# Performance work log

Measured on AMD Instinct MI355X. Metric: run time of the kernel, lower is better.

The kernel has to match this reference:

```python
import itertools
import jax, jax.numpy as jnp
import numpy as np

B, RES = 256, 16
DIM, KEY_DIM, NUM_HEADS, ATTN_RATIO = 448, 32, 8, 4
SEQ = RES * RES
EXP_KEY_DIM = ATTN_RATIO * KEY_DIM          # 128
TOTAL_KEY = KEY_DIM * NUM_HEADS             # 256
TOTAL_EXP = EXP_KEY_DIM * NUM_HEADS         # 1024
QKV_DIM = TOTAL_EXP + 2 * TOTAL_KEY         # 1536
SCALE = KEY_DIM ** -0.5


def _build_bias_idxs():
    # Replicates the itertools.product loop from build()
    points = list(itertools.product(range(RES), range(RES)))
    offsets = {}
    idxs = []
    for p1 in points:
        for p2 in points:
            off = (abs(p1[0] - p2[0]), abs(p1[1] - p2[1]))
            if off not in offsets:
                offsets[off] = len(offsets)
            idxs.append(offsets[off])
    return np.asarray(idxs, dtype=np.int32).reshape(SEQ, SEQ), len(offsets)


def setup_inputs() -> dict:
    key = jax.random.key(0)
    ks = jax.random.split(key, 6)
    bias_idxs_np, n_off = _build_bias_idxs()
    std = 0.02
    return {
        "hidden_states": jax.random.normal(ks[0], (B, SEQ, DIM), dtype=jnp.float32),
        "qkv_w": jax.random.normal(ks[1], (DIM, QKV_DIM), dtype=jnp.float32) * std,
        "qkv_b": jnp.zeros((QKV_DIM,), dtype=jnp.float32),
        "proj_w": jax.random.normal(ks[2], (TOTAL_EXP, DIM), dtype=jnp.float32) * std,
        "proj_b": jnp.zeros((DIM,), dtype=jnp.float32),
        "attention_biases": jax.random.normal(ks[3], (NUM_HEADS, n_off), dtype=jnp.float32) * std,
        "attention_bias_idxs": jnp.asarray(bias_idxs_np),
    }


def reference(hidden_states, qkv_w, qkv_b, proj_w, proj_b, attention_biases, attention_bias_idxs):
    b, s, _ = hidden_states.shape
    qkv = hidden_states @ qkv_w + qkv_b                       # [B,S,1536]
    qkv = qkv.reshape(b, s, NUM_HEADS, KEY_DIM * 2 + EXP_KEY_DIM)
    q, k, v = jnp.split(qkv, [KEY_DIM, 2 * KEY_DIM], axis=3)  # [B,S,H,dk],[B,S,H,dk],[B,S,H,dv]
    scores = jnp.einsum("bqhd,bkhd->bhqk", q, k) * SCALE      # [B,H,S,S]
    bias = attention_biases[:, attention_bias_idxs]           # [H,S,S] gather
    probs = jax.nn.softmax(scores + bias[None], axis=-1)
    ctx = jnp.einsum("bhqk,bkhd->bqhd", probs, v)             # [B,S,H,dv]
    ctx = ctx.reshape(b, s, TOTAL_EXP)
    return ctx @ proj_w + proj_b
```

## Files before the change

### kernel.cpp

```cpp
#include <hip/hip_runtime.h>
#include <hip/hip_bf16.h>
#include <stdint.h>


typedef __attribute__((ext_vector_type(4))) float f32x4;
typedef __attribute__((ext_vector_type(8))) short short8;
typedef __attribute__((ext_vector_type(4))) unsigned short u16x4;
typedef __attribute__((ext_vector_type(2))) unsigned int u32x2;

#define DEVINL static __device__ __forceinline__

DEVINL unsigned short f2bf(float f) {
  unsigned u = __float_as_uint(f);
  return (unsigned short)((u + 0x7FFFu + ((u >> 16) & 1u)) >> 16);
}
DEVINL float bf2f(short s) {
  return __uint_as_float(((unsigned)(unsigned short)s) << 16);
}
DEVINL unsigned cvt_pk_bf16(float lo, float hi) {
  unsigned r;
  asm("v_cvt_pk_bf16_f32 %0, %1, %2" : "=v"(r) : "v"(lo), "v"(hi));
  return r;
}

DEVINL void gload_lds16(const void* g, void* l) {
  __builtin_amdgcn_global_load_lds((const __attribute__((address_space(1))) void*)g,
                                   (__attribute__((address_space(3))) void*)l,
                                   16, 0, 0);
}

#define SCALE 0.17677669529663687f
#define LOG2E 1.4426950408889634f

#define WS_XB     ((size_t)0)
#define WS_CTX    ((size_t)0)
#define WS_WQT    ((size_t)134217728)
#define WS_WPT    ((size_t)135593984)
#define WS_QW     ((size_t)136642560)
#define WS_KW     ((size_t)170196992)
#define WS_VT     ((size_t)203751424)
#define WS_QKVBP  ((size_t)342163456)

DEVINL int qkv_perm(int np, float* sc) {
  *sc = 1.0f;
  if (np < 512) {
    const int h = np >> 6, c = np & 63;
    if (c < 32) *sc = SCALE * LOG2E;
    return h * 192 + c;
  }
  const int h = (np - 512) >> 7, e = (np - 512) & 127;
  return h * 192 + 64 + e;
}


__global__ void k_convert_x(const float* __restrict__ x, short* __restrict__ xb) {
  const size_t i = (size_t)blockIdx.x * blockDim.x + threadIdx.x;
  const f32x4* src = (const f32x4*)x + i * 2;
  f32x4 a = src[0], b = src[1];
  short8 o;
#pragma unroll
  for (int t = 0; t < 4; ++t) o[t] = (short)f2bf(a[t]);
#pragma unroll
  for (int t = 0; t < 4; ++t) o[4 + t] = (short)f2bf(b[t]);
  ((short8*)xb)[i] = o;
}

__global__ void k_prep_qkvw(const float* __restrict__ w, short* __restrict__ out) {
  const int idx = blockIdx.x * blockDim.x + threadIdx.x;
  if (idx >= 1536 * 448) return;
  const int np = idx / 448, k = idx - np * 448;
  float sc;
  const int n = qkv_perm(np, &sc);
  out[idx] = (short)f2bf(w[(size_t)k * 1536 + n] * sc);
}

__global__ void k_prep_qkvb(const float* __restrict__ bsrc, float* __restrict__ bdst) {
  const int np = blockIdx.x * blockDim.x + threadIdx.x;
  if (np >= 1536) return;
  float sc;
  const int n = qkv_perm(np, &sc);
  bdst[np] = bsrc[n] * sc;
}

__global__ void k_transpose_bf16(const float* __restrict__ in, short* __restrict__ out,
                                 int K, int N, int total) {
  const int idx = blockIdx.x * blockDim.x + threadIdx.x;
  if (idx >= total) return;
  const int n = idx / K, k = idx - n * K;
  const float v = (n < N) ? in[(size_t)k * N + n] : 0.0f;
  out[idx] = (short)f2bf(v);
}


template <int KSTEPS, int LDA, int LDB, bool SWAP>
DEVINL void gemm128_pipe3(const short* __restrict__ A, const short* __restrict__ B,
                          short* Asm , short* Bsm ,
                          int m0, int n0, int tid, f32x4 acc[4][4]) {
  const int lane = tid & 63, wave = tid >> 6;
  const int l15 = lane & 15, g = lane >> 4;
  const int wm = wave >> 1, wn = wave & 1;
  const int r8 = lane >> 3;
  const int scol = (((lane & 7) ^ r8) << 3);
  const int wbase = wave * 32;

  const short* Ab = A + (size_t)(m0 + wbase + r8) * LDA + scol;
  const short* Bb = B + (size_t)(n0 + wbase + r8) * LDB + scol;

  auto stageA = [&](int k) {
    short* dst = Asm + (k % 3) * 8192 + wbase * 64;
    const short* src = Ab + (size_t)k * 64;
#pragma unroll
    for (int c = 0; c < 4; ++c) gload_lds16(src + (size_t)(c * 8) * LDA, dst + c * 512);
  };
  auto stageB = [&](int k) {
    short* dst = Bsm + (k % 2) * 8192 + wbase * 64;
    const short* src = Bb + (size_t)k * 64;
#pragma unroll
    for (int c = 0; c < 4; ++c) gload_lds16(src + (size_t)(c * 8) * LDB, dst + c * 512);
  };
  auto compute = [&](int k) {
    const short* Ac = Asm + (k % 3) * 8192;
    const short* Bc = Bsm + (k % 2) * 8192;
#pragma unroll
    for (int s = 0; s < 2; ++s) {
      const int rslot = (((s * 4 + g) ^ (l15 & 7)) << 3);
      short8 a[4], b[4];
#pragma unroll
      for (int i = 0; i < 4; ++i)
        a[i] = *(const short8*)(Ac + (wm * 64 + i * 16 + l15) * 64 + rslot);
#pragma unroll
      for (int j = 0; j < 4; ++j)
        b[j] = *(const short8*)(Bc + (wn * 64 + j * 16 + l15) * 64 + rslot);
#pragma unroll
      for (int i = 0; i < 4; ++i)
#pragma unroll
        for (int j = 0; j < 4; ++j)
          acc[i][j] = SWAP
              ? __builtin_amdgcn_mfma_f32_16x16x32_bf16(b[j], a[i], acc[i][j], 0, 0, 0)
              : __builtin_amdgcn_mfma_f32_16x16x32_bf16(a[i], b[j], acc[i][j], 0, 0, 0);
    }
  };

  stageB(0); stageA(0); stageA(1);
  asm volatile("s_waitcnt vmcnt(4)" ::: "memory");
  __builtin_amdgcn_s_barrier();
  __builtin_amdgcn_sched_barrier(0);

#pragma unroll
  for (int ks = 0; ks < KSTEPS - 2; ++ks) {
    stageB(ks + 1);
    stageA(ks + 2);
    asm volatile("s_waitcnt vmcnt(12)" ::: "memory");
    __builtin_amdgcn_s_barrier();
    __builtin_amdgcn_sched_barrier(0);
    compute(ks);
    __builtin_amdgcn_s_barrier();
  }
  stageB(KSTEPS - 1);
  asm volatile("s_waitcnt vmcnt(8)" ::: "memory");
  __builtin_amdgcn_s_barrier();
  __builtin_amdgcn_sched_barrier(0);
  compute(KSTEPS - 2);
  __builtin_amdgcn_s_barrier();
  asm volatile("s_waitcnt vmcnt(0)" ::: "memory");
  __builtin_amdgcn_s_barrier();
  __builtin_amdgcn_sched_barrier(0);
  compute(KSTEPS - 1);
}


union QkvSmem {
  struct { short a[3 * 8192]; short b[2 * 8192]; } ab;
  short tile[128 * 136];
};

__global__ __launch_bounds__(256) void k_qkv_gemm(
    const short* __restrict__ Xb, const short* __restrict__ Wt,
    const float* __restrict__ qkvbp,
    short* __restrict__ Qw, short* __restrict__ Kw, short* __restrict__ Vt) {
  __shared__ __align__(16) QkvSmem sm;
  const int tid = threadIdx.x;
  const int l = (blockIdx.x & 7) * 768 + (blockIdx.x >> 3);
  const int mt = l / 12, by = l - mt * 12;
  const int m0 = mt * 128, n0 = by * 128;

  const int lane = tid & 63, wave = tid >> 6;
  const int l15 = lane & 15, g = lane >> 4;
  const int wm = wave >> 1, wn = wave & 1;
  const int b0 = m0 >> 8, s0 = m0 & 255;

  f32x4 acc[4][4];
#pragma unroll
  for (int i = 0; i < 4; ++i)
#pragma unroll
    for (int j = 0; j < 4; ++j) acc[i][j] = (f32x4){0.f, 0.f, 0.f, 0.f};

  if (by >= 4) {
    gemm128_pipe3<7, 448, 448, false>(Xb, Wt, sm.ab.a, sm.ab.b, m0, n0, tid, acc);
    __syncthreads();
#pragma unroll
    for (int i = 0; i < 4; ++i) {
#pragma unroll
      for (int j = 0; j < 4; ++j) {
        const float bv = qkvbp[n0 + wn * 64 + j * 16 + l15];
        u16x4 pk;
#pragma unroll
        for (int r = 0; r < 4; ++r) pk[r] = f2bf(acc[i][j][r] + bv);
        *(u16x4*)&sm.tile[(wn * 64 + j * 16 + l15) * 136 + wm * 64 + i * 16 + g * 4] = pk;
      }
    }
    __syncthreads();
    const int bh = b0 * 8 + (by - 4);
#pragma unroll
    for (int p = 0; p < 8; ++p) {
      const int er = p * 16 + (tid >> 4);
      const int sc = (tid & 15) * 8;
      short8 v = *(const short8*)&sm.tile[er * 136 + sc];
      *(short8*)(Vt + (size_t)bh * 33792 + er * 264 + s0 + sc) = v;
    }
  } else {
    gemm128_pipe3<7, 448, 448, true>(Xb, Wt, sm.ab.a, sm.ab.b, m0, n0, tid, acc);
#pragma unroll
    for (int i = 0; i < 4; ++i) {
      const int s = s0 + wm * 64 + i * 16 + l15;
#pragma unroll
      for (int j = 0; j < 4; ++j) {
        const int nbase = n0 + wn * 64 + j * 16 + g * 4;
        const f32x4 bv4 = *(const f32x4*)(qkvbp + nbase);
        u16x4 pk;
#pragma unroll
        for (int r = 0; r < 4; ++r) pk[r] = f2bf(acc[i][j][r] + bv4[r]);
        const int c = nbase & 63;
        const int bh = b0 * 8 + (by << 1) + (nbase >> 6 & 1);
        short* dst = (c < 32) ? (Qw + ((size_t)bh * 256 + s) * 32 + c)
                              : (Kw + ((size_t)bh * 256 + s) * 32 + (c - 32));
        *(u16x4*)dst = pk;
      }
    }
  }
}


__global__ __launch_bounds__(512, 4) void k_attn(
    const short* __restrict__ Qw, const short* __restrict__ Kw,
    const short* __restrict__ Vt, const float* __restrict__ attb, int n_off,
    short* __restrict__ CTX) {
  __shared__ short Ps[4][32 * 264];
  __shared__ float rinv[2][4][32];
  __shared__ float bias_sm[256];

  const int tid = threadIdx.x, lane = tid & 63, wave = tid >> 6;
  const int l15 = lane & 15, g = lane >> 4;
  const int bh = blockIdx.x;
  const int b = bh >> 3, h = bh & 7;

  if (tid < 256) bias_sm[tid] = attb[h * n_off + tid] * LOG2E;
  __syncthreads();

  int offc[4];
#pragma unroll
  for (int r = 0; r < 4; ++r) {
    const int d = g * 4 + r - l15;
    offc[r] = (d < 0) ? -d : d;
  }

  const short* Qb = Qw + (size_t)bh * 8192;
  const short* Kb = Kw + (size_t)bh * 8192;
  const short* Vb = Vt + (size_t)bh * 33792;
  const int e = wave * 16 + l15;

  for (int ph = 0; ph < 2; ++ph) {
    const int Q0 = ph * 128;

    short8 aq[4][2];
#pragma unroll
    for (int u = 0; u < 4; ++u)
#pragma unroll
      for (int i = 0; i < 2; ++i)
        aq[u][i] = *(const short8*)(Qb + (Q0 + u * 32 + i * 16 + l15) * 32 + g * 8);
    short8 bkk[2];
#pragma unroll
    for (int fj = 0; fj < 2; ++fj)
      bkk[fj] = *(const short8*)(Kb + (wave * 32 + fj * 16 + l15) * 32 + g * 8);
    short8 bvv[8];
#pragma unroll
    for (int ks = 0; ks < 8; ++ks)
      bvv[ks] = *(const short8*)(Vb + e * 264 + ks * 32 + g * 8);

#pragma unroll
    for (int fj = 0; fj < 2; ++fj) {
      const int kk0 = wave * 32 + fj * 16;
      const int kr = wave * 2 + fj;
#pragma unroll
      for (int u = 0; u < 4; ++u) {
#pragma unroll
        for (int i = 0; i < 2; ++i) {
          const int qr = ph * 8 + u * 2 + i;
          const int ab = ((qr > kr) ? qr - kr : kr - qr) << 4;
          f32x4 acc;
#pragma unroll
          for (int r = 0; r < 4; ++r) acc[r] = bias_sm[ab + offc[r]];
          acc = __builtin_amdgcn_mfma_f32_16x16x32_bf16(bkk[fj], aq[u][i], acc, 0, 0, 0);
          u32x2 pk;
          pk.x = cvt_pk_bf16(exp2f(acc[0]), exp2f(acc[1]));
          pk.y = cvt_pk_bf16(exp2f(acc[2]), exp2f(acc[3]));
          *(u32x2*)&Ps[u][(i * 16 + l15) * 264 + kk0 + g * 4] = pk;
        }
      }
    }
    __syncthreads();

    {
      const int r = tid >> 4, part = tid & 15;
#pragma unroll
      for (int u = 0; u < 4; ++u) {
        const short* rowp = &Ps[u][r * 264 + part * 16];
        short8 x0 = ((const short8*)rowp)[0];
        short8 x1 = ((const short8*)rowp)[1];
        float sum = 0.f;
#pragma unroll
        for (int t = 0; t < 8; ++t) sum += bf2f(x0[t]) + bf2f(x1[t]);
#pragma unroll
        for (int d = 1; d < 16; d <<= 1) sum += __shfl_xor(sum, d);
        if (part == 0) rinv[ph][u][r] = 1.0f / sum;
      }
    }

    f32x4 cacc[4][2];
#pragma unroll
    for (int u = 0; u < 4; ++u)
#pragma unroll
      for (int qt = 0; qt < 2; ++qt) cacc[u][qt] = (f32x4){0.f, 0.f, 0.f, 0.f};

#pragma unroll
    for (int ks = 0; ks < 8; ++ks) {
#pragma unroll
      for (int u = 0; u < 4; ++u)
#pragma unroll
        for (int qt = 0; qt < 2; ++qt) {
          const short8 ap = *(const short8*)&Ps[u][(qt * 16 + l15) * 264 + ks * 32 + g * 8];
          cacc[u][qt] = __builtin_amdgcn_mfma_f32_16x16x32_bf16(ap, bvv[ks], cacc[u][qt], 0, 0, 0);
        }
    }
    __syncthreads();

#pragma unroll
    for (int u = 0; u < 4; ++u)
#pragma unroll
      for (int qt = 0; qt < 2; ++qt) {
        const int qb = qt * 16 + g * 4;
        const size_t base = ((size_t)b * 256 + Q0 + u * 32 + qb) * 1024 + h * 128 + wave * 16 + l15;
#pragma unroll
        for (int r = 0; r < 4; r += 2) {
          const unsigned pw = cvt_pk_bf16(cacc[u][qt][r] * rinv[ph][u][qb + r],
                                          cacc[u][qt][r + 1] * rinv[ph][u][qb + r + 1]);
          CTX[base + (size_t)r * 1024] = (short)(pw & 0xffffu);
          CTX[base + (size_t)(r + 1) * 1024] = (short)(pw >> 16);
        }
      }
  }
}


__global__ __launch_bounds__(256) void k_proj_gemm(
    const short* __restrict__ CTX, const short* __restrict__ Wpt,
    const float* __restrict__ projb, float* __restrict__ out) {
  __shared__ __align__(16) short Asm[3 * 8192];
  __shared__ __align__(16) short Bsm[2 * 8192];
  const int tid = threadIdx.x;
  const int l = (blockIdx.x & 7) * 256 + (blockIdx.x >> 3);
  const int mt = l >> 2, nt = l & 3;
  const int m0 = mt * 128, n0 = nt * 128;
  f32x4 acc[4][4];
#pragma unroll
  for (int i = 0; i < 4; ++i)
#pragma unroll
    for (int j = 0; j < 4; ++j) acc[i][j] = (f32x4){0.f, 0.f, 0.f, 0.f};

  gemm128_pipe3<16, 1024, 1024, false>(CTX, Wpt, Asm, Bsm, m0, n0, tid, acc);

  const int lane = tid & 63, wave = tid >> 6;
  const int l15 = lane & 15, g = lane >> 4;
  const int wm = wave >> 1, wn = wave & 1;
#pragma unroll
  for (int i = 0; i < 4; ++i) {
    const int mb = m0 + wm * 64 + i * 16 + g * 4;
#pragma unroll
    for (int j = 0; j < 4; ++j) {
      const int n = n0 + wn * 64 + j * 16 + l15;
      if (n < 448) {
        const float bv = projb[n];
#pragma unroll
        for (int r = 0; r < 4; ++r)
          out[(size_t)(mb + r) * 448 + n] = acc[i][j][r] + bv;
      }
    }
  }
}


extern "C" void kernel_launch(void* const* d_in, const int* in_sizes, int n_in,
                              void* d_out, int out_size, void* d_ws, size_t ws_size,
                              hipStream_t stream) {
  const float* X      = (const float*)d_in[0];
  const float* qkv_w  = (const float*)d_in[1];
  const float* qkv_b  = (const float*)d_in[2];
  const float* proj_w = (const float*)d_in[3];
  const float* proj_b = (const float*)d_in[4];
  const float* att_b  = (const float*)d_in[5];
  const int n_off = in_sizes[5] / 8;

  char* ws = (char*)d_ws;
  short* Xb    = (short*)(ws + WS_XB);
  short* CTX   = (short*)(ws + WS_CTX);
  short* WQT   = (short*)(ws + WS_WQT);
  short* WPT   = (short*)(ws + WS_WPT);
  short* Qw    = (short*)(ws + WS_QW);
  short* Kw    = (short*)(ws + WS_KW);
  short* Vt    = (short*)(ws + WS_VT);
  float* QKVBP = (float*)(ws + WS_QKVBP);

  k_convert_x<<<14336, 256, 0, stream>>>(X, Xb);
  k_prep_qkvw<<<(1536 * 448 + 255) / 256, 256, 0, stream>>>(qkv_w, WQT);
  k_prep_qkvb<<<6, 256, 0, stream>>>(qkv_b, QKVBP);
  k_transpose_bf16<<<(512 * 1024 + 255) / 256, 256, 0, stream>>>(proj_w, WPT, 1024, 448, 512 * 1024);

  k_qkv_gemm<<<6144, 256, 0, stream>>>(Xb, WQT, QKVBP, Qw, Kw, Vt);
  k_attn<<<2048, 512, 0, stream>>>(Qw, Kw, Vt, att_b, n_off, CTX);
  k_proj_gemm<<<2048, 256, 0, stream>>>(CTX, WPT, proj_b, (float*)d_out);
}
```

Before: 360.0 us.

## Rewrite projection GEMM with 256x256 tiles, 8 waves, quadrant-interleaved pipeline

The output projection GEMM moves from 128x128 tiles on 256 threads to 256x256 tiles on 512 threads. Each tile is split into four 128x128 quadrants, and the loads of the next k-step's halves are interleaved with MFMA work on the current quadrants using explicit vmcnt waits and barriers. The bigger tile is meant to raise operand reuse per LDS byte and cut global traffic. In exchange it wastes more work on the 448-wide N dimension (512 padded columns) and uses 128KB of LDS. Scheduling barriers are also added to the shared stage helpers, which changes codegen for the QKV GEMM too.

```diff
diff --git a/kernel.cpp b/kernel.cpp
--- a/kernel.cpp
+++ b/kernel.cpp
@@ -111,12 +111,14 @@
     const short* src = Ab + (size_t)k * 64;
 #pragma unroll
     for (int c = 0; c < 4; ++c) gload_lds16(src + (size_t)(c * 8) * LDA, dst + c * 512);
+    __builtin_amdgcn_sched_barrier(0);
   };
   auto stageB = [&](int k) {
     short* dst = Bsm + (k % 2) * 8192 + wbase * 64;
     const short* src = Bb + (size_t)k * 64;
 #pragma unroll
     for (int c = 0; c < 4; ++c) gload_lds16(src + (size_t)(c * 8) * LDB, dst + c * 512);
+    __builtin_amdgcn_sched_barrier(0);
   };
   auto compute = [&](int k) {
     const short* Ac = Asm + (k % 3) * 8192;
@@ -362,40 +364,151 @@
 }
 
 
-__global__ __launch_bounds__(256) void k_proj_gemm(
+__global__ __launch_bounds__(512, 2) void k_proj_gemm(
     const short* __restrict__ CTX, const short* __restrict__ Wpt,
     const float* __restrict__ projb, float* __restrict__ out) {
-  __shared__ __align__(16) short Asm[3 * 8192];
-  __shared__ __align__(16) short Bsm[2 * 8192];
-  const int tid = threadIdx.x;
-  const int l = (blockIdx.x & 7) * 256 + (blockIdx.x >> 3);
-  const int mt = l >> 2, nt = l & 3;
-  const int m0 = mt * 128, n0 = nt * 128;
-  f32x4 acc[4][4];
-#pragma unroll
-  for (int i = 0; i < 4; ++i)
-#pragma unroll
-    for (int j = 0; j < 4; ++j) acc[i][j] = (f32x4){0.f, 0.f, 0.f, 0.f};
-
-  gemm128_pipe3<16, 1024, 1024, false>(CTX, Wpt, Asm, Bsm, m0, n0, tid, acc);
-
-  const int lane = tid & 63, wave = tid >> 6;
+  __shared__ __align__(16) short Ab[2][2 * 8192];
+  __shared__ __align__(16) short Bb[2][2 * 8192];
+
+  const int tid = threadIdx.x, lane = tid & 63, wave = tid >> 6;
   const int l15 = lane & 15, g = lane >> 4;
-  const int wm = wave >> 1, wn = wave & 1;
-#pragma unroll
-  for (int i = 0; i < 4; ++i) {
-    const int mb = m0 + wm * 64 + i * 16 + g * 4;
-#pragma unroll
-    for (int j = 0; j < 4; ++j) {
-      const int n = n0 + wn * 64 + j * 16 + l15;
-      if (n < 448) {
-        const float bv = projb[n];
-#pragma unroll
-        for (int r = 0; r < 4; ++r)
-          out[(size_t)(mb + r) * 448 + n] = acc[i][j][r] + bv;
-      }
-    }
-  }
+  const int l = (blockIdx.x & 7) * 64 + (blockIdx.x >> 3);
+  const int mt = l >> 1, nt = l & 1;
+  const int m0 = mt * 256, n0 = nt * 256;
+
+  const int fmB = (wave & 3) * 2;
+  const int fnB = (wave >> 2) * 4;
+
+  const int r8 = lane >> 3;
+  const int scol = (((lane & 7) ^ r8) << 3);
+
+  const short* Asrc = CTX + (size_t)m0 * 1024 + scol;
+  const short* Bsrc = Wpt + (size_t)n0 * 1024 + scol;
+
+  auto stageA = [&](int kt, int half) {
+    short* dst = &Ab[kt & 1][half * 8192];
+#pragma unroll
+    for (int c = 0; c < 2; ++c) {
+      const int row0 = c * 64 + wave * 8;
+      gload_lds16(Asrc + (size_t)(half * 128 + row0 + r8) * 1024 + kt * 64,
+                  dst + row0 * 64);
+    }
+    __builtin_amdgcn_sched_barrier(0);
+  };
+  auto stageB = [&](int kt, int half) {
+    short* dst = &Bb[kt & 1][half * 8192];
+#pragma unroll
+    for (int c = 0; c < 2; ++c) {
+      const int row0 = c * 64 + wave * 8;
+      gload_lds16(Bsrc + (size_t)(half * 128 + row0 + r8) * 1024 + kt * 64,
+                  dst + row0 * 64);
+    }
+    __builtin_amdgcn_sched_barrier(0);
+  };
+
+  f32x4 acc[2][2][2][4];
+#pragma unroll
+  for (int a = 0; a < 2; ++a)
+#pragma unroll
+    for (int bq = 0; bq < 2; ++bq)
+#pragma unroll
+      for (int i = 0; i < 2; ++i)
+#pragma unroll
+        for (int j = 0; j < 4; ++j) acc[a][bq][i][j] = (f32x4){0.f, 0.f, 0.f, 0.f};
+
+  short8 Ar[2][2][2];
+  short8 Br[4][2];
+
+  auto readA = [&](int par, int hm) {
+    const short* base = &Ab[par][hm * 8192];
+#pragma unroll
+    for (int fi = 0; fi < 2; ++fi)
+#pragma unroll
+      for (int ks = 0; ks < 2; ++ks)
+        Ar[hm][fi][ks] = *(const short8*)(base + ((fmB + fi) * 16 + l15) * 64 +
+                                          (((ks * 4 + g) ^ (l15 & 7)) << 3));
+  };
+  auto readB = [&](int par, int hn) {
+    const short* base = &Bb[par][hn * 8192];
+#pragma unroll
+    for (int fi = 0; fi < 4; ++fi)
+#pragma unroll
+      for (int ks = 0; ks < 2; ++ks)
+        Br[fi][ks] = *(const short8*)(base + ((fnB + fi) * 16 + l15) * 64 +
+                                      (((ks * 4 + g) ^ (l15 & 7)) << 3));
+  };
+  auto mfmaQ = [&](int hm, int hn) {
+#pragma unroll
+    for (int ks = 0; ks < 2; ++ks)
+#pragma unroll
+      for (int fi = 0; fi < 2; ++fi)
+#pragma unroll
+        for (int fj = 0; fj < 4; ++fj)
+          acc[hm][hn][fi][fj] = __builtin_amdgcn_mfma_f32_16x16x32_bf16(
+              Ar[hm][fi][ks], Br[fj][ks], acc[hm][hn][fi][fj], 0, 0, 0);
+  };
+
+  stageA(0, 0); stageB(0, 0); stageA(0, 1); stageB(0, 1);
+
+  for (int T = 0; T < 15; ++T) {
+    const int par = T & 1;
+    stageA(T + 1, 0);
+    asm volatile("s_waitcnt vmcnt(6)" ::: "memory");
+    __builtin_amdgcn_s_barrier();
+    __builtin_amdgcn_sched_barrier(0);
+    readA(par, 0); readB(par, 0);
+    mfmaQ(0, 0);
+    stageB(T + 1, 0);
+    asm volatile("s_waitcnt vmcnt(6)" ::: "memory");
+    __builtin_amdgcn_s_barrier();
+    __builtin_amdgcn_sched_barrier(0);
+    readA(par, 1);
+    mfmaQ(1, 0);
+    stageA(T + 1, 1);
+    asm volatile("s_waitcnt vmcnt(6)" ::: "memory");
+    __builtin_amdgcn_s_barrier();
+    __builtin_amdgcn_sched_barrier(0);
+    readB(par, 1);
+    mfmaQ(1, 1);
+    stageB(T + 1, 1);
+    mfmaQ(0, 1);
+  }
+  {
+    asm volatile("s_waitcnt vmcnt(4)" ::: "memory");
+    __builtin_amdgcn_s_barrier();
+    __builtin_amdgcn_sched_barrier(0);
+    readA(1, 0); readB(1, 0);
+    mfmaQ(0, 0);
+    asm volatile("s_waitcnt vmcnt(2)" ::: "memory");
+    __builtin_amdgcn_s_barrier();
+    __builtin_amdgcn_sched_barrier(0);
+    readA(1, 1);
+    mfmaQ(1, 0);
+    asm volatile("s_waitcnt vmcnt(0)" ::: "memory");
+    __builtin_amdgcn_s_barrier();
+    __builtin_amdgcn_sched_barrier(0);
+    readB(1, 1);
+    mfmaQ(1, 1);
+    mfmaQ(0, 1);
+  }
+
+#pragma unroll
+  for (int hm = 0; hm < 2; ++hm)
+#pragma unroll
+    for (int hn = 0; hn < 2; ++hn)
+#pragma unroll
+      for (int fi = 0; fi < 2; ++fi)
+#pragma unroll
+        for (int fj = 0; fj < 4; ++fj) {
+          const int n = n0 + hn * 128 + (fnB + fj) * 16 + l15;
+          if (n < 448) {
+            const float bv = projb[n];
+            const int mb = m0 + hm * 128 + (fmB + fi) * 16 + g * 4;
+#pragma unroll
+            for (int r = 0; r < 4; ++r)
+              out[(size_t)(mb + r) * 448 + n] = acc[hm][hn][fi][fj][r] + bv;
+          }
+        }
 }
 
 
@@ -427,5 +540,5 @@
 
   k_qkv_gemm<<<6144, 256, 0, stream>>>(Xb, WQT, QKVBP, Qw, Kw, Vt);
   k_attn<<<2048, 512, 0, stream>>>(Qw, Kw, Vt, att_b, n_off, CTX);
-  k_proj_gemm<<<2048, 256, 0, stream>>>(CTX, WPT, proj_b, (float*)d_out);
-}
+  k_proj_gemm<<<512, 512, 0, stream>>>(CTX, WPT, proj_b, (float*)d_out);
+}
```

Result: faster. 334.9 us (-7.0%).
